# Optimization experiments

Hardware: AMD Instinct MI355X
Metric: run time of the kernel (lower is better)

Reference implementation:

```python
import jax, jax.numpy as jnp
import numpy as np

D_IN = 1024
D_OUT = 1024
NUM_HEADS = 16
D_HEAD = D_OUT // NUM_HEADS


def setup_inputs() -> dict:
    key = jax.random.key(0)
    ks = jax.random.split(key, 6)
    s = 0.02
    return {
        "x": jax.random.normal(ks[0], (2, 2048, D_IN), dtype=jnp.float32),
        "W_q": jax.random.normal(ks[1], (D_IN, D_OUT), dtype=jnp.float32) * s,
        "W_k": jax.random.normal(ks[2], (D_IN, D_OUT), dtype=jnp.float32) * s,
        "W_v": jax.random.normal(ks[3], (D_IN, D_OUT), dtype=jnp.float32) * s,
        "W_o": jax.random.normal(ks[4], (D_OUT, D_OUT), dtype=jnp.float32) * s,
        "b_o": jax.random.normal(ks[5], (D_OUT,), dtype=jnp.float32) * s,
    }


def reference(x, W_q, W_k, W_v, W_o, b_o):
    B, T, _ = x.shape
    # qkv projections (no bias), split heads -> [B, H, T, d_head]
    def split_heads(t):
        return t.reshape(B, T, NUM_HEADS, D_HEAD).transpose(0, 2, 1, 3)
    q = split_heads(x @ W_q)
    k = split_heads(x @ W_k)
    v = split_heads(x @ W_v)
    # full causal scores [B, H, T, T]
    scores = jnp.einsum("bhqd,bhkd->bhqk", q, k)
    causal = jnp.triu(jnp.ones((T, T), dtype=bool), k=1)
    scores = jnp.where(causal, -jnp.inf, scores)
    attn = jax.nn.softmax(scores / np.sqrt(D_HEAD).astype(np.float32), axis=-1)
    # dropout rate is 0.0 -> identity
    ctx = jnp.einsum("bhqk,bhkd->bhqd", attn, v)
    ctx = ctx.transpose(0, 2, 1, 3).reshape(B, T, D_OUT)
    return ctx @ W_o + b_o
```

## Files before the change

kernel.cpp:

```cpp
#include <hip/hip_runtime.h>
#include <hip/hip_bf16.h>
#include <cstdint>

#define SEQ_T 2048
#define DMODEL 1024
#define NHEAD 16
#define DHEAD 64

typedef __attribute__((ext_vector_type(8))) __bf16 bf16x8;
typedef __attribute__((ext_vector_type(4))) float floatx4;
typedef __attribute__((ext_vector_type(16))) float floatx16;
typedef __attribute__((ext_vector_type(2))) unsigned uint32x2;

static __device__ __forceinline__ uint16_t f2bf(float f) {
    union { float f; uint32_t u; } v; v.f = f;
    uint32_t r = v.u + 0x7FFFu + ((v.u >> 16) & 1u);
    return (uint16_t)(r >> 16);
}

static __device__ __forceinline__ uint32_t pack2bf(float a, float b) {
    union { __bf16 h[2]; uint32_t u; } p;
    p.h[0] = (__bf16)a; p.h[1] = (__bf16)b;
    return p.u;
}

__global__ void mha_cvt(const float* __restrict__ x, uint16_t* __restrict__ xb,
                        const float* __restrict__ W0, const float* __restrict__ W1,
                        const float* __restrict__ W2, const float* __restrict__ W3,
                        uint16_t* __restrict__ T0, uint16_t* __restrict__ T1,
                        uint16_t* __restrict__ T2, uint16_t* __restrict__ T3) {
    if (blockIdx.z == 4) {
        int base = (blockIdx.y * 16 + blockIdx.x) * 256 + threadIdx.x;
#pragma unroll
        for (int i = 0; i < 16; ++i) {
            int idx = base + i * 65536;
            float4 f = ((const float4*)x)[idx];
            union { uint16_t u[4]; uint64_t v; } o;
            o.u[0] = f2bf(f.x); o.u[1] = f2bf(f.y); o.u[2] = f2bf(f.z); o.u[3] = f2bf(f.w);
            ((uint64_t*)xb)[idx] = o.v;
        }
        return;
    }
    const float* W; uint16_t* Tt; float sc;
    switch (blockIdx.z) {
        case 0: W = W0; Tt = T0; sc = 0.125f * 1.44269504089f; break;
        case 1: W = W1; Tt = T1; sc = 1.f; break;
        case 2: W = W2; Tt = T2; sc = 1.f; break;
        default: W = W3; Tt = T3; sc = 1.f; break;
    }
    __shared__ float tile[64][65];
    const int c  = threadIdx.x & 63;
    const int r0 = threadIdx.x >> 6;
    const int R0 = blockIdx.y * 64, C0 = blockIdx.x * 64;
#pragma unroll
    for (int rr = 0; rr < 16; ++rr) {
        int r = r0 + rr * 4;
        tile[r][c] = W[(size_t)(R0 + r) * DMODEL + C0 + c];
    }
    __syncthreads();
#pragma unroll
    for (int rr = 0; rr < 16; ++rr) {
        int r = r0 + rr * 4;
        Tt[(size_t)(C0 + r) * DMODEL + R0 + c] = f2bf(tile[c][r] * sc);
    }
}

template<int MODE>
__device__ __forceinline__ void gemm_bk64_body(
    const uint16_t* __restrict__ A, const uint16_t* __restrict__ Bt,
    uint16_t* __restrict__ outB) {
    const int K = DMODEL, N = DMODEL;
    extern __shared__ char smem[];
    uint16_t* As = (uint16_t*)smem;
    uint16_t* Bs = (uint16_t*)(smem + 8192);
    const int tid  = threadIdx.x;
    const int wave = tid >> 6;
    const int lane = tid & 63;
    const int m0 = blockIdx.y * 64;
    const int n0 = blockIdx.x * 128;
    const int lr   = lane & 15;
    const int quad = lane >> 4;

    floatx4 acc[4][2];
#pragma unroll
    for (int i = 0; i < 4; ++i)
#pragma unroll
        for (int j = 0; j < 2; ++j) acc[i][j] = (floatx4)0.0f;

    for (int k0 = 0; k0 < K; k0 += 64) {
#pragma unroll
        for (int i = 0; i < 2; ++i) {
            int c = i * 256 + tid;
            int r = c >> 3, s = (c & 7) ^ (r & 7);
            const uint16_t* g = A + (size_t)(m0 + r) * K + k0 + s * 8;
            __builtin_amdgcn_global_load_lds((const __attribute__((address_space(1))) void*)g,
                                             (__attribute__((address_space(3))) void*)(As + (size_t)c * 8), 16, 0, 0);
        }
#pragma unroll
        for (int i = 0; i < 4; ++i) {
            int c = i * 256 + tid;
            int r = c >> 3, s = (c & 7) ^ (r & 7);
            const uint16_t* g = Bt + (size_t)(n0 + r) * K + k0 + s * 8;
            __builtin_amdgcn_global_load_lds((const __attribute__((address_space(1))) void*)g,
                                             (__attribute__((address_space(3))) void*)(Bs + (size_t)c * 8), 16, 0, 0);
        }
        __syncthreads();
#pragma unroll
        for (int ks = 0; ks < 2; ++ks) {
            bf16x8 af[4], bfr[2];
#pragma unroll
            for (int mi = 0; mi < 4; ++mi) {
                int row = mi * 16 + lr;
                af[mi] = *(const bf16x8*)&As[row * 64 + (((ks * 4 + quad) ^ (row & 7)) << 3)];
            }
#pragma unroll
            for (int ni = 0; ni < 2; ++ni) {
                int row = wave * 32 + ni * 16 + lr;
                bfr[ni] = *(const bf16x8*)&Bs[row * 64 + (((ks * 4 + quad) ^ (row & 7)) << 3)];
            }
#pragma unroll
            for (int mi = 0; mi < 4; ++mi)
#pragma unroll
                for (int ni = 0; ni < 2; ++ni)
                    acc[mi][ni] = __builtin_amdgcn_mfma_f32_16x16x32_bf16(af[mi], bfr[ni], acc[mi][ni], 0, 0, 0);
        }
        __syncthreads();
    }
    if constexpr (MODE == 1) {
        uint16_t* Ct = (uint16_t*)smem;
        const int bb = m0 >> 11, t0 = m0 & 2047;
#pragma unroll
        for (int mi = 0; mi < 4; ++mi)
#pragma unroll
            for (int ni = 0; ni < 2; ++ni) {
                int cl = wave * 32 + ni * 16 + lr;
                int tl = mi * 16 + quad * 4;
                int tls = tl ^ ((cl & 3) << 4);
                union { uint16_t u[4]; uint64_t v8; } pk;
#pragma unroll
                for (int r = 0; r < 4; ++r) pk.u[r] = f2bf(acc[mi][ni][r]);
                *(uint64_t*)&Ct[cl * 72 + tls] = pk.v8;
            }
        __syncthreads();
#pragma unroll
        for (int k = 0; k < 4; ++k) {
            int c = k * 256 + tid;
            int cl = c >> 3, off = (c & 7) * 8;
            int offs = off ^ ((cl & 3) << 4);
            uint4 v = *(const uint4*)&Ct[cl * 72 + offs];
            *(uint4*)&outB[((size_t)(bb * 1024 + n0 + cl)) * 2048 + t0 + off] = v;
        }
    } else {
#pragma unroll
        for (int mi = 0; mi < 4; ++mi)
#pragma unroll
            for (int ni = 0; ni < 2; ++ni) {
                int col = n0 + wave * 32 + ni * 16 + lr;
#pragma unroll
                for (int r = 0; r < 4; ++r) {
                    int row = m0 + mi * 16 + quad * 4 + r;
                    outB[(size_t)row * N + col] = f2bf(acc[mi][ni][r]);
                }
            }
    }
}

__global__ __launch_bounds__(256) void mha_gemm_qkv(
    const uint16_t* __restrict__ A,
    const uint16_t* __restrict__ Wq, const uint16_t* __restrict__ Wk, const uint16_t* __restrict__ Wv,
    uint16_t* __restrict__ Q, uint16_t* __restrict__ K, uint16_t* __restrict__ Vt) {
    switch (blockIdx.z) {
        case 0:  gemm_bk64_body<0>(A, Wq, Q);  break;
        case 1:  gemm_bk64_body<0>(A, Wk, K);  break;
        default: gemm_bk64_body<1>(A, Wv, Vt); break;
    }
}

__global__ __launch_bounds__(512) void mha_gemm_out(
    const uint16_t* __restrict__ A, const uint16_t* __restrict__ Wot,
    float* __restrict__ out, const float* __restrict__ bias) {
    const int K = DMODEL, N = DMODEL;
    extern __shared__ char smem[];
    uint16_t* As = (uint16_t*)smem;
    uint16_t* Bs = (uint16_t*)(smem + 8192);
    const int tid  = threadIdx.x;
    const int wave = tid >> 6;
    const int lane = tid & 63;
    const int m0 = blockIdx.y * 64;
    const int n0 = blockIdx.x * 128;
    const int lr   = lane & 15;
    const int quad = lane >> 4;
    const int wm = wave >> 2, wn = wave & 3;

    floatx4 acc[2][2];
#pragma unroll
    for (int i = 0; i < 2; ++i)
#pragma unroll
        for (int j = 0; j < 2; ++j) acc[i][j] = (floatx4)0.0f;

    for (int k0 = 0; k0 < K; k0 += 64) {
        {
            int c = tid;
            int r = c >> 3, s = (c & 7) ^ (r & 7);
            const uint16_t* g = A + (size_t)(m0 + r) * K + k0 + s * 8;
            __builtin_amdgcn_global_load_lds((const __attribute__((address_space(1))) void*)g,
                                             (__attribute__((address_space(3))) void*)(As + (size_t)c * 8), 16, 0, 0);
        }
#pragma unroll
        for (int i = 0; i < 2; ++i) {
            int c = i * 512 + tid;
            int r = c >> 3, s = (c & 7) ^ (r & 7);
            const uint16_t* g = Wot + (size_t)(n0 + r) * K + k0 + s * 8;
            __builtin_amdgcn_global_load_lds((const __attribute__((address_space(1))) void*)g,
                                             (__attribute__((address_space(3))) void*)(Bs + (size_t)c * 8), 16, 0, 0);
        }
        __syncthreads();
#pragma unroll
        for (int ks = 0; ks < 2; ++ks) {
            bf16x8 af[2], bfr[2];
#pragma unroll
            for (int mi = 0; mi < 2; ++mi) {
                int row = wm * 32 + mi * 16 + lr;
                af[mi] = *(const bf16x8*)&As[row * 64 + (((ks * 4 + quad) ^ (row & 7)) << 3)];
            }
#pragma unroll
            for (int ni = 0; ni < 2; ++ni) {
                int row = wn * 32 + ni * 16 + lr;
                bfr[ni] = *(const bf16x8*)&Bs[row * 64 + (((ks * 4 + quad) ^ (row & 7)) << 3)];
            }
#pragma unroll
            for (int mi = 0; mi < 2; ++mi)
#pragma unroll
                for (int ni = 0; ni < 2; ++ni)
                    acc[mi][ni] = __builtin_amdgcn_mfma_f32_16x16x32_bf16(af[mi], bfr[ni], acc[mi][ni], 0, 0, 0);
        }
        __syncthreads();
    }
#pragma unroll
    for (int mi = 0; mi < 2; ++mi)
#pragma unroll
        for (int ni = 0; ni < 2; ++ni) {
            int col = n0 + wn * 32 + ni * 16 + lr;
            float bv = bias[col];
#pragma unroll
            for (int r = 0; r < 4; ++r) {
                int row = m0 + wm * 32 + mi * 16 + quad * 4 + r;
                out[(size_t)row * N + col] = acc[mi][ni][r] + bv;
            }
        }
}

__global__ __launch_bounds__(512, 2) void mha_attn_mfma(
    const uint16_t* __restrict__ Q, const uint16_t* __restrict__ K,
    const uint16_t* __restrict__ Vt, uint16_t* __restrict__ ctx) {
    __shared__ alignas(16) uint16_t Ks[2][128 * 64];
    __shared__ float lbuf[256];

    const int tid  = threadIdx.x;
    const int wave = tid >> 6;
    const int lane = tid & 63;
    const int l31  = lane & 31;
    const int hi   = lane >> 5;
    const int l7   = lane & 7;
    const int qg   = wave & 1;
    const int kvq  = wave >> 1;
    const int h = blockIdx.x;
    const int p = blockIdx.y;
    const int b = blockIdx.z;
    const int jH = 31 - p, jL = p;
    const int TH = (33 - p) >> 1;

    const uint16_t* kg[2];
    int cch[2];
#pragma unroll
    for (int i = 0; i < 2; ++i) {
        int c = i * 512 + tid; cch[i] = c;
        int rk = c >> 3, ck = c & 7;
        kg[i] = K + ((size_t)(b * SEQ_T) + rk) * DMODEL + h * DHEAD + ((ck ^ (rk & 7)) * 8);
    }
    const uint16_t* Vg = Vt + ((size_t)(b * 1024 + h * DHEAD)) * 2048;

    int q0w = jH * 64 + qg * 32;
    bf16x8 qf[4];
    auto load_q = [&]() {
        const uint16_t* qb = Q + ((size_t)(b * SEQ_T) + q0w + l31) * DMODEL + h * DHEAD;
#pragma unroll
        for (int f = 0; f < 4; ++f)
            qf[f] = *(const bf16x8*)(qb + f * 16 + hi * 8);
    };
    load_q();

    floatx16 o[2];
#pragma unroll
    for (int dt = 0; dt < 2; ++dt) o[dt] = (floatx16)0.0f;
    float lac = 0.f;

    auto stage = [&](int kv0, int buf) {
#pragma unroll
        for (int i = 0; i < 2; ++i)
            __builtin_amdgcn_global_load_lds(
                (const __attribute__((address_space(1))) void*)(kg[i] + (size_t)kv0 * DMODEL),
                (__attribute__((address_space(3))) void*)(&Ks[buf][cch[i] * 8]), 16, 0, 0);
    };

    auto halfsum = [&](float x) -> float {
#if __has_builtin(__builtin_amdgcn_permlane32_swap)
        uint32x2 r = __builtin_amdgcn_permlane32_swap(__float_as_uint(x), __float_as_uint(x), false, false);
        return __uint_as_float(r.x) + __uint_as_float(r.y);
#else
        return x + __shfl_xor(x, 32, 64);
#endif
    };

    auto combine_store = [&](int cur) {
        __syncthreads();
        float* osc = (float*)&Ks[cur][0];
        float lt = halfsum(lac);
#pragma unroll
        for (int pass = 3; pass >= 1; --pass) {
            if (kvq == pass) {
                if (pass == 3) {
#pragma unroll
                    for (int dt = 0; dt < 2; ++dt)
#pragma unroll
                        for (int r = 0; r < 16; ++r) {
                            int row = (r & 3) + 8 * (r >> 2) + 4 * hi;
                            osc[(qg * 32 + row) * 64 + dt * 32 + l31] = o[dt][r];
                        }
                    if (lane < 32) lbuf[qg * 32 + lane] = lt;
                } else {
#pragma unroll
                    for (int dt = 0; dt < 2; ++dt)
#pragma unroll
                        for (int r = 0; r < 16; ++r) {
                            int row = (r & 3) + 8 * (r >> 2) + 4 * hi;
                            osc[(qg * 32 + row) * 64 + dt * 32 + l31] += o[dt][r];
                        }
                    if (lane < 32) lbuf[qg * 32 + lane] += lt;
                }
            }
            __syncthreads();
        }
        if (kvq == 0) {
            float ltot = lt + lbuf[qg * 32 + l31];
            if (lane < 32) lbuf[64 + qg * 32 + lane] = 1.f / ltot;
#pragma unroll
            for (int dt = 0; dt < 2; ++dt)
#pragma unroll
                for (int r = 0; r < 16; ++r) {
                    int row = (r & 3) + 8 * (r >> 2) + 4 * hi;
                    float ov = o[dt][r] + osc[(qg * 32 + row) * 64 + dt * 32 + l31];
                    float li = lbuf[64 + qg * 32 + row];
                    size_t addr = ((size_t)(b * SEQ_T) + q0w + row) * DMODEL + h * DHEAD + dt * 32 + l31;
                    ctx[addr] = f2bf(ov * li);
                }
        }
    };

    stage(0, 0);
    __syncthreads();

    for (int t = 0; t < 17; ++t) {
        const int cur = t & 1;
        const int kv0 = (t < TH ? t : t - TH) * 128;
        if (t + 1 < 17) {
            int tn = t + 1;
            stage((tn < TH ? tn : tn - TH) * 128, tn & 1);
        }
        const int kb = kv0 + kvq * 32;
        floatx16 s = (floatx16)0.0f;
        __builtin_amdgcn_s_setprio(1);
#pragma unroll
        for (int f = 0; f < 4; ++f) {
            bf16x8 kf = *(const bf16x8*)&Ks[cur][(kvq * 32 + l31) * 64 + (((2 * f + hi) ^ l7) << 3)];
            s = __builtin_amdgcn_mfma_f32_32x32x16_bf16(kf, qf[f], s, 0, 0, 0);
        }
        __builtin_amdgcn_s_setprio(0);
        if (kb + 31 > q0w) {
            int qr = q0w + l31;
#pragma unroll
            for (int r = 0; r < 16; ++r) {
                int k = kb + (r & 3) + 8 * (r >> 2) + 4 * hi;
                if (k > qr) s[r] = -3e38f;
            }
        }
        uint32_t d0[2], d1[2], d2[2], d3[2];
#pragma unroll
        for (int i = 0; i < 2; ++i) {
            float a, c2;
            a = __builtin_amdgcn_exp2f(s[2 * i]);      c2 = __builtin_amdgcn_exp2f(s[2 * i + 1]);
            lac += a + c2; d0[i] = pack2bf(a, c2);
            a = __builtin_amdgcn_exp2f(s[4 + 2 * i]);  c2 = __builtin_amdgcn_exp2f(s[4 + 2 * i + 1]);
            lac += a + c2; d1[i] = pack2bf(a, c2);
            a = __builtin_amdgcn_exp2f(s[8 + 2 * i]);  c2 = __builtin_amdgcn_exp2f(s[8 + 2 * i + 1]);
            lac += a + c2; d2[i] = pack2bf(a, c2);
            a = __builtin_amdgcn_exp2f(s[12 + 2 * i]); c2 = __builtin_amdgcn_exp2f(s[12 + 2 * i + 1]);
            lac += a + c2; d3[i] = pack2bf(a, c2);
        }
        bf16x8 paf[2];
#if __has_builtin(__builtin_amdgcn_permlane32_swap)
        {
            uint32x2 r0 = __builtin_amdgcn_permlane32_swap(d0[0], d1[0], false, false);
            uint32x2 r1 = __builtin_amdgcn_permlane32_swap(d0[1], d1[1], false, false);
            union { uint32_t u[4]; bf16x8 v; } f0;
            f0.u[0] = r0.x; f0.u[1] = r1.x; f0.u[2] = r0.y; f0.u[3] = r1.y;
            paf[0] = f0.v;
            uint32x2 r2 = __builtin_amdgcn_permlane32_swap(d2[0], d3[0], false, false);
            uint32x2 r3 = __builtin_amdgcn_permlane32_swap(d2[1], d3[1], false, false);
            union { uint32_t u[4]; bf16x8 v; } f1;
            f1.u[0] = r2.x; f1.u[1] = r3.x; f1.u[2] = r2.y; f1.u[3] = r3.y;
            paf[1] = f1.v;
        }
#else
        {
            uint32_t s00 = __shfl_xor((int)d0[0], 32, 64), s01 = __shfl_xor((int)d0[1], 32, 64);
            uint32_t s10 = __shfl_xor((int)d1[0], 32, 64), s11 = __shfl_xor((int)d1[1], 32, 64);
            union { uint32_t u[4]; bf16x8 v; } f0;
            f0.u[0] = hi ? s10 : d0[0]; f0.u[1] = hi ? s11 : d0[1];
            f0.u[2] = hi ? d1[0] : s00; f0.u[3] = hi ? d1[1] : s01;
            paf[0] = f0.v;
            uint32_t s20 = __shfl_xor((int)d2[0], 32, 64), s21 = __shfl_xor((int)d2[1], 32, 64);
            uint32_t s30 = __shfl_xor((int)d3[0], 32, 64), s31 = __shfl_xor((int)d3[1], 32, 64);
            union { uint32_t u[4]; bf16x8 v; } f1;
            f1.u[0] = hi ? s30 : d2[0]; f1.u[1] = hi ? s31 : d2[1];
            f1.u[2] = hi ? d3[0] : s20; f1.u[3] = hi ? d3[1] : s21;
            paf[1] = f1.v;
        }
#endif
        __builtin_amdgcn_s_setprio(1);
#pragma unroll
        for (int f = 0; f < 2; ++f)
#pragma unroll
            for (int dt = 0; dt < 2; ++dt) {
                bf16x8 vf = *(const bf16x8*)&Vg[(size_t)(dt * 32 + l31) * 2048 + kv0 + ((kvq * 4 + 2 * f + hi) * 8)];
                o[dt] = __builtin_amdgcn_mfma_f32_32x32x16_bf16(paf[f], vf, o[dt], 0, 0, 0);
            }
        __builtin_amdgcn_s_setprio(0);
        if (t == TH - 1) {
            combine_store(cur);
            q0w = jL * 64 + qg * 32;
            load_q();
#pragma unroll
            for (int dt = 0; dt < 2; ++dt) o[dt] = (floatx16)0.0f;
            lac = 0.f;
        }
        if (t + 1 < 17) __syncthreads();
    }
    combine_store(0);
}

extern "C" void kernel_launch(void* const* d_in, const int* in_sizes, int n_in,
                              void* d_out, int out_size, void* d_ws, size_t ws_size,
                              hipStream_t stream) {
    const float* x  = (const float*)d_in[0];
    const float* Wq = (const float*)d_in[1];
    const float* Wk = (const float*)d_in[2];
    const float* Wv = (const float*)d_in[3];
    const float* Wo = (const float*)d_in[4];
    const float* bo = (const float*)d_in[5];
    float* out = (float*)d_out;

    char* ws = (char*)d_ws;
    const size_t SZ_X = (size_t)4096 * DMODEL * 2;
    const size_t SZ_W = (size_t)DMODEL * DMODEL * 2;
    size_t off = 0;
    uint16_t* xb  = (uint16_t*)(ws + off); off += SZ_X;
    uint16_t* wqt = (uint16_t*)(ws + off); off += SZ_W;
    uint16_t* wkt = (uint16_t*)(ws + off); off += SZ_W;
    uint16_t* wvt = (uint16_t*)(ws + off); off += SZ_W;
    uint16_t* wot = (uint16_t*)(ws + off); off += SZ_W;
    uint16_t* Qb  = (uint16_t*)(ws + off); off += SZ_X;
    uint16_t* Kb  = (uint16_t*)(ws + off); off += SZ_X;
    uint16_t* Vtb = (uint16_t*)(ws + off); off += SZ_X;
    uint16_t* Cb  = (uint16_t*)(ws + off); off += SZ_X;
    (void)ws_size; (void)in_sizes; (void)n_in; (void)out_size;

    mha_cvt<<<dim3(16, 16, 5), 256, 0, stream>>>(x, xb, Wq, Wk, Wv, Wo, wqt, wkt, wvt, wot);
    mha_gemm_qkv<<<dim3(8, 64, 3), 256, 24576, stream>>>(xb, wqt, wkt, wvt, Qb, Kb, Vtb);
    mha_attn_mfma<<<dim3(NHEAD, 16, 2), 512, 0, stream>>>(Qb, Kb, Vtb, Cb);
    mha_gemm_out<<<dim3(8, 64), 512, 24576, stream>>>(Cb, wot, out, bo);
}
```

Before: 204.2 us.

## Enlarge attention blocks to 128 query rows and stage V tiles through LDS

The attention kernel now uses 1024-thread blocks covering 128 query rows per pair (16 waves, 4 query groups × 4 KV quarters) and halves the grid. V tiles are now loaded asynchronously into swizzled LDS alongside K, instead of being read directly from global memory inside the PV loop. This doubles K/V reuse per staged tile and hides V fetch latency. The cost is 65KB of dynamic LDS and larger blocks, which cuts blocks per CU and leaves fewer blocks for load balancing.

```diff
diff --git a/kernel.cpp b/kernel.cpp
--- a/kernel.cpp
+++ b/kernel.cpp
@@ -250,11 +250,13 @@
         }
 }
 
-__global__ __launch_bounds__(512, 2) void mha_attn_mfma(
+__global__ __launch_bounds__(1024) void mha_attn_mfma(
     const uint16_t* __restrict__ Q, const uint16_t* __restrict__ K,
     const uint16_t* __restrict__ Vt, uint16_t* __restrict__ ctx) {
-    __shared__ alignas(16) uint16_t Ks[2][128 * 64];
-    __shared__ float lbuf[256];
+    extern __shared__ char asmem[];
+    uint16_t* Ks0 = (uint16_t*)asmem;
+    uint16_t* Vs0 = (uint16_t*)(asmem + 32768);
+    float*    lbuf = (float*)(asmem + 65536);
 
     const int tid  = threadIdx.x;
     const int wave = tid >> 6;
@@ -262,25 +264,26 @@
     const int l31  = lane & 31;
     const int hi   = lane >> 5;
     const int l7   = lane & 7;
-    const int qg   = wave & 1;
-    const int kvq  = wave >> 1;
+    const int qg   = wave & 3;
+    const int kvq  = wave >> 2;
     const int h = blockIdx.x;
     const int p = blockIdx.y;
     const int b = blockIdx.z;
-    const int jH = 31 - p, jL = p;
-    const int TH = (33 - p) >> 1;
-
-    const uint16_t* kg[2];
-    int cch[2];
-#pragma unroll
-    for (int i = 0; i < 2; ++i) {
-        int c = i * 512 + tid; cch[i] = c;
+    const int jH = 15 - p, jL = p;
+    const int TH = jH + 1;
+
+    const uint16_t* kg;
+    const uint16_t* vg;
+    {
+        int c = tid;
         int rk = c >> 3, ck = c & 7;
-        kg[i] = K + ((size_t)(b * SEQ_T) + rk) * DMODEL + h * DHEAD + ((ck ^ (rk & 7)) * 8);
-    }
-    const uint16_t* Vg = Vt + ((size_t)(b * 1024 + h * DHEAD)) * 2048;
-
-    int q0w = jH * 64 + qg * 32;
+        kg = K + ((size_t)(b * SEQ_T) + rk) * DMODEL + h * DHEAD + ((ck ^ (rk & 7)) * 8);
+        int rv = c >> 4, cv = c & 15;
+        int sv = (cv & 8) | ((cv & 7) ^ (rv & 7));
+        vg = Vt + ((size_t)(b * 1024 + h * DHEAD + rv)) * 2048 + sv * 8;
+    }
+
+    int q0w = jH * 128 + qg * 32;
     bf16x8 qf[4];
     auto load_q = [&]() {
         const uint16_t* qb = Q + ((size_t)(b * SEQ_T) + q0w + l31) * DMODEL + h * DHEAD;
@@ -296,11 +299,12 @@
     float lac = 0.f;
 
     auto stage = [&](int kv0, int buf) {
-#pragma unroll
-        for (int i = 0; i < 2; ++i)
-            __builtin_amdgcn_global_load_lds(
-                (const __attribute__((address_space(1))) void*)(kg[i] + (size_t)kv0 * DMODEL),
-                (__attribute__((address_space(3))) void*)(&Ks[buf][cch[i] * 8]), 16, 0, 0);
+        __builtin_amdgcn_global_load_lds(
+            (const __attribute__((address_space(1))) void*)(kg + (size_t)kv0 * DMODEL),
+            (__attribute__((address_space(3))) void*)(Ks0 + buf * 8192 + tid * 8), 16, 0, 0);
+        __builtin_amdgcn_global_load_lds(
+            (const __attribute__((address_space(1))) void*)(vg + kv0),
+            (__attribute__((address_space(3))) void*)(Vs0 + buf * 8192 + tid * 8), 16, 0, 0);
     };
 
     auto halfsum = [&](float x) -> float {
@@ -314,7 +318,9 @@
 
     auto combine_store = [&](int cur) {
         __syncthreads();
-        float* osc = (float*)&Ks[cur][0];
+        float* osc = (qg < 2) ? (float*)(Ks0 + cur * 8192)
+                              : (float*)(Vs0 + cur * 8192);
+        const int qoff = (qg & 1) * 32;
         float lt = halfsum(lac);
 #pragma unroll
         for (int pass = 3; pass >= 1; --pass) {
@@ -325,7 +331,7 @@
 #pragma unroll
                         for (int r = 0; r < 16; ++r) {
                             int row = (r & 3) + 8 * (r >> 2) + 4 * hi;
-                            osc[(qg * 32 + row) * 64 + dt * 32 + l31] = o[dt][r];
+                            osc[(qoff + row) * 64 + dt * 32 + l31] = o[dt][r];
                         }
                     if (lane < 32) lbuf[qg * 32 + lane] = lt;
                 } else {
@@ -334,7 +340,7 @@
 #pragma unroll
                         for (int r = 0; r < 16; ++r) {
                             int row = (r & 3) + 8 * (r >> 2) + 4 * hi;
-                            osc[(qg * 32 + row) * 64 + dt * 32 + l31] += o[dt][r];
+                            osc[(qoff + row) * 64 + dt * 32 + l31] += o[dt][r];
                         }
                     if (lane < 32) lbuf[qg * 32 + lane] += lt;
                 }
@@ -343,14 +349,14 @@
         }
         if (kvq == 0) {
             float ltot = lt + lbuf[qg * 32 + l31];
-            if (lane < 32) lbuf[64 + qg * 32 + lane] = 1.f / ltot;
+            if (lane < 32) lbuf[128 + qg * 32 + lane] = 1.f / ltot;
 #pragma unroll
             for (int dt = 0; dt < 2; ++dt)
 #pragma unroll
                 for (int r = 0; r < 16; ++r) {
                     int row = (r & 3) + 8 * (r >> 2) + 4 * hi;
-                    float ov = o[dt][r] + osc[(qg * 32 + row) * 64 + dt * 32 + l31];
-                    float li = lbuf[64 + qg * 32 + row];
+                    float ov = o[dt][r] + osc[(qoff + row) * 64 + dt * 32 + l31];
+                    float li = lbuf[128 + qg * 32 + row];
                     size_t addr = ((size_t)(b * SEQ_T) + q0w + row) * DMODEL + h * DHEAD + dt * 32 + l31;
                     ctx[addr] = f2bf(ov * li);
                 }
@@ -367,12 +373,14 @@
             int tn = t + 1;
             stage((tn < TH ? tn : tn - TH) * 128, tn & 1);
         }
+        const uint16_t* Kc = Ks0 + cur * 8192;
+        const uint16_t* Vc = Vs0 + cur * 8192;
         const int kb = kv0 + kvq * 32;
         floatx16 s = (floatx16)0.0f;
         __builtin_amdgcn_s_setprio(1);
 #pragma unroll
         for (int f = 0; f < 4; ++f) {
-            bf16x8 kf = *(const bf16x8*)&Ks[cur][(kvq * 32 + l31) * 64 + (((2 * f + hi) ^ l7) << 3)];
+            bf16x8 kf = *(const bf16x8*)&Kc[(kvq * 32 + l31) * 64 + (((2 * f + hi) ^ l7) << 3)];
             s = __builtin_amdgcn_mfma_f32_32x32x16_bf16(kf, qf[f], s, 0, 0, 0);
         }
         __builtin_amdgcn_s_setprio(0);
@@ -432,13 +440,13 @@
         for (int f = 0; f < 2; ++f)
 #pragma unroll
             for (int dt = 0; dt < 2; ++dt) {
-                bf16x8 vf = *(const bf16x8*)&Vg[(size_t)(dt * 32 + l31) * 2048 + kv0 + ((kvq * 4 + 2 * f + hi) * 8)];
+                bf16x8 vf = *(const bf16x8*)&Vc[(dt * 32 + l31) * 128 + (((kvq * 4 + 2 * f + hi) ^ l7) << 3)];
                 o[dt] = __builtin_amdgcn_mfma_f32_32x32x16_bf16(paf[f], vf, o[dt], 0, 0, 0);
             }
         __builtin_amdgcn_s_setprio(0);
         if (t == TH - 1) {
             combine_store(cur);
-            q0w = jL * 64 + qg * 32;
+            q0w = jL * 128 + qg * 32;
             load_q();
 #pragma unroll
             for (int dt = 0; dt < 2; ++dt) o[dt] = (floatx16)0.0f;
@@ -477,6 +485,6 @@
 
     mha_cvt<<<dim3(16, 16, 5), 256, 0, stream>>>(x, xb, Wq, Wk, Wv, Wo, wqt, wkt, wvt, wot);
     mha_gemm_qkv<<<dim3(8, 64, 3), 256, 24576, stream>>>(xb, wqt, wkt, wvt, Qb, Kb, Vtb);
-    mha_attn_mfma<<<dim3(NHEAD, 16, 2), 512, 0, stream>>>(Qb, Kb, Vtb, Cb);
+    mha_attn_mfma<<<dim3(NHEAD, 8, 2), 1024, 66560, stream>>>(Qb, Kb, Vtb, Cb);
     mha_gemm_out<<<dim3(8, 64), 512, 24576, stream>>>(Cb, wot, out, bo);
 }
```

New measurement: 181.0 us. 11.4% less time.
